# Performance work log

Measured on AMD Instinct MI355X. Metric: run time of the kernel, lower is better.

Reference implementation:

```python
import jax, jax.numpy as jnp
import numpy as np

TIME = 4096
DIM = 2048
DT_TAU = 0.1 / 1.0  # dt / tau


def setup_inputs() -> dict:
    key = jax.random.key(0)
    k1, k2, k3, k4 = jax.random.split(key, 4)
    inputs = jax.random.normal(k1, (TIME, 1, DIM), dtype=jnp.float32)
    W = jax.random.normal(k2, (DIM, DIM), dtype=jnp.float32) * 0.02  # recurrent weight (nn.Linear, bias=False)
    bias = jax.random.normal(k3, (1, DIM), dtype=jnp.float32)
    initial = jax.random.normal(k4, (1, DIM), dtype=jnp.float32)
    return {"inputs": inputs, "W": W, "bias": bias, "initial": initial}


def reference(inputs, W, bias, initial):
    # states[0] = initial; states[t+1] = s*(1-dt/tau) + (dt/tau)*(sigmoid(s+bias)@W.T + inputs[t])
    def step(state, x_t):
        f = jax.nn.sigmoid(state + bias) @ W.T  # [1, dim]
        new_state = state * (1.0 - DT_TAU) + DT_TAU * (f + x_t)
        return new_state, new_state

    _, rest = jax.lax.scan(step, initial, inputs[: TIME - 1])  # rest: [time-1, 1, dim]
    return jnp.concatenate([initial[None], rest], axis=0)  # [time, 1, dim]
```

## Files before the change

### kernel.cpp

```cpp
#include <hip/hip_runtime.h>
#include <hip/hip_fp16.h>
#include <hip/hip_cooperative_groups.h>
#include <stdint.h>

#define TIME_STEPS 4096
#define DIM        2048
#define NBLK       256
#define NTH        512
#define NWORK      32
#define WVB        8
#define RPW        8
#define PITCH      132

typedef uint32_t u32x4 __attribute__((ext_vector_type(4)));
typedef _Float16 h2f16 __attribute__((ext_vector_type(2)));


__device__ __forceinline__ uint32_t umin32(uint32_t a, uint32_t b) { return a < b ? a : b; }

__device__ __forceinline__ float dot2f(uint32_t packed, h2f16 w, float acc) {
#if __has_builtin(__builtin_amdgcn_fdot2)
  return __builtin_amdgcn_fdot2(__builtin_bit_cast(h2f16, packed), w, acc, false);
#else
  h2f16 a = __builtin_bit_cast(h2f16, packed);
  acc = fmaf((float)a.x, (float)w.x, acc);
  return fmaf((float)a.y, (float)w.y, acc);
#endif
}

template<int NSLOT>
__global__ __launch_bounds__(NTH, 2) void ctrnn_kernel(
    const float* __restrict__ x,
    const float* __restrict__ W,
    const float* __restrict__ bias,
    const float* __restrict__ initial,
    float* __restrict__ out,
    uint32_t* __restrict__ actbuf,
    uint32_t* __restrict__ progress,
    uint32_t* __restrict__ xccmap)
{
  const int tid  = threadIdx.x;
  const int lane = tid & 63;
  const int wv   = tid >> 6;

  if (tid == 0) {
    uint32_t xcc;
    asm volatile("s_getreg_b32 %0, hwreg(HW_REG_XCC_ID)" : "=s"(xcc));
    __hip_atomic_store(&xccmap[blockIdx.x], xcc,
                       __ATOMIC_RELAXED, __HIP_MEMORY_SCOPE_AGENT);
  }
  cooperative_groups::this_grid().sync();

  __shared__ uint32_t s_map[NBLK];
  for (int i = tid; i < NBLK; i += NTH)
    s_map[i] = __hip_atomic_load(&xccmap[i], __ATOMIC_RELAXED, __HIP_MEMORY_SCOPE_AGENT);
  __syncthreads();
  const uint32_t target = s_map[0];
  int before = 0, total = 0, beforeN = 0;
  const int bid = blockIdx.x;
  for (int i = 0; i < NBLK; ++i) {
    const bool m = (s_map[i] == target);
    total += m;
    if (i < bid) { before += m; beforeN += !m; }
  }
  const bool mine = (s_map[bid] == target);
  const int rank = mine ? before : (total + beforeN);
  if (rank >= NWORK) return;
  const int wb = rank;

  __shared__ uint32_t lds[2][16 * PITCH];

  const int gwid = wb * WVB + wv;
  const int row0 = gwid * RPW;

  const int s_c = lane >> 2, rr = lane & 3;
  const int cb  = s_c * 128 + rr * 4;
  h2f16 w2[RPW][16];
  #pragma unroll
  for (int m = 0; m < RPW; ++m) {
    const float* wr = W + (size_t)(row0 + m) * DIM + cb;
    #pragma unroll
    for (int k = 0; k < 8; ++k) {
      w2[m][2*k]   = h2f16{(_Float16)wr[k*16 + 0], (_Float16)wr[k*16 + 1]};
      w2[m][2*k+1] = h2f16{(_Float16)wr[k*16 + 2], (_Float16)wr[k*16 + 3]};
    }
  }

  float v = 0.f, bj = 0.f, xv = 0.f, xw = 0.f;
  if (lane < RPW) {
    const int j = row0 + lane;
    v  = initial[j];
    bj = bias[j];
    xv = x[j];
    xw = x[DIM + j];
    out[j] = v;
    const float a0 = 1.0f / (1.0f + __expf(-(v + bj)));
    __half h = __float2half_rn(a0);
    uint16_t hb; __builtin_memcpy(&hb, &h, 2);
    __hip_atomic_store(&actbuf[j], (1u << 16) | hb,
                       __ATOMIC_RELAXED, __HIP_MEMORY_SCOPE_AGENT);
  }

  const int e0   = wv * 256 + lane * 4;
  const int dstw = (e0 >> 7) * PITCH + (e0 & 127);

  uint32_t prog_seen = 0;

  for (int t = 0; t < TIME_STEPS - 1; ++t) {
    const int b = t & 1;
    const uint32_t needtag = (uint32_t)(t + 1);
    const uint32_t thresh  = needtag << 16;

    const uint32_t* qsrc = actbuf + (size_t)(t & (NSLOT - 1)) * DIM + e0;
    u32x4 q;
    for (;;) {
      asm volatile("global_load_dwordx4 %0, %1, off sc1\n\t"
                   "s_waitcnt vmcnt(0)"
                   : "=v"(q) : "v"(qsrc) : "memory");
      const uint32_t mn = umin32(umin32(q[0], q[1]), umin32(q[2], q[3]));
      if (mn >= thresh) break;
    }
    *reinterpret_cast<u32x4*>(&lds[b][dstw]) = q;

    __syncthreads();

    if (tid == 0)
      __hip_atomic_store(&progress[wb], needtag,
                         __ATOMIC_RELAXED, __HIP_MEMORY_SCOPE_AGENT);

    float xn = 0.f;
    if (lane < RPW && t + 2 < TIME_STEPS) xn = x[(size_t)(t + 2) * DIM + row0 + lane];

    float a0 = 0.f, a1 = 0.f, a2 = 0.f, a3 = 0.f;
    float a4 = 0.f, a5 = 0.f, a6 = 0.f, a7 = 0.f;
    #pragma unroll
    for (int k = 0; k < 8; ++k) {
      const u32x4 qq = *reinterpret_cast<const u32x4*>(
          &lds[b][s_c * PITCH + rr * 4 + k * 16]);
      const uint32_t lo = __builtin_amdgcn_perm(qq[1], qq[0], 0x05040100u);
      const uint32_t hi = __builtin_amdgcn_perm(qq[3], qq[2], 0x05040100u);
      a0 = dot2f(lo, w2[0][2*k], a0); a0 = dot2f(hi, w2[0][2*k+1], a0);
      a1 = dot2f(lo, w2[1][2*k], a1); a1 = dot2f(hi, w2[1][2*k+1], a1);
      a2 = dot2f(lo, w2[2][2*k], a2); a2 = dot2f(hi, w2[2][2*k+1], a2);
      a3 = dot2f(lo, w2[3][2*k], a3); a3 = dot2f(hi, w2[3][2*k+1], a3);
      a4 = dot2f(lo, w2[4][2*k], a4); a4 = dot2f(hi, w2[4][2*k+1], a4);
      a5 = dot2f(lo, w2[5][2*k], a5); a5 = dot2f(hi, w2[5][2*k+1], a5);
      a6 = dot2f(lo, w2[6][2*k], a6); a6 = dot2f(hi, w2[6][2*k+1], a6);
      a7 = dot2f(lo, w2[7][2*k], a7); a7 = dot2f(hi, w2[7][2*k+1], a7);
    }

    const float t0 = a0 + __shfl_xor(a0, 1, 64);
    const float t1 = a1 + __shfl_xor(a1, 1, 64);
    const float t2 = a2 + __shfl_xor(a2, 1, 64);
    const float t3 = a3 + __shfl_xor(a3, 1, 64);
    const float t4 = a4 + __shfl_xor(a4, 1, 64);
    const float t5 = a5 + __shfl_xor(a5, 1, 64);
    const float t6 = a6 + __shfl_xor(a6, 1, 64);
    const float t7 = a7 + __shfl_xor(a7, 1, 64);
    float b0 = (lane & 1) ? t1 : t0;
    float b1 = (lane & 1) ? t3 : t2;
    float b2 = (lane & 1) ? t5 : t4;
    float b3 = (lane & 1) ? t7 : t6;
    b0 += __shfl_xor(b0, 2, 64);
    b1 += __shfl_xor(b1, 2, 64);
    b2 += __shfl_xor(b2, 2, 64);
    b3 += __shfl_xor(b3, 2, 64);
    float c0 = (lane & 2) ? b1 : b0;
    float c1 = (lane & 2) ? b3 : b2;
    c0 += __shfl_xor(c0, 4, 64);
    c1 += __shfl_xor(c1, 4, 64);
    float p = (lane & 4) ? c1 : c0;
    p += __shfl_xor(p, 8, 64);
    p += __shfl_xor(p, 16, 64);
    p += __shfl_xor(p, 32, 64);

    if (t >= NSLOT - 1) {
      const uint32_t need = (uint32_t)(t + 2 - NSLOT);
      if (need > prog_seen) {
        for (;;) {
          uint32_t mn = __hip_atomic_load(&progress[lane & (NWORK - 1)],
                            __ATOMIC_RELAXED, __HIP_MEMORY_SCOPE_AGENT);
          uint32_t qv;
          qv = (uint32_t)__shfl_xor((int)mn, 1, 64);  mn = umin32(mn, qv);
          qv = (uint32_t)__shfl_xor((int)mn, 2, 64);  mn = umin32(mn, qv);
          qv = (uint32_t)__shfl_xor((int)mn, 4, 64);  mn = umin32(mn, qv);
          qv = (uint32_t)__shfl_xor((int)mn, 8, 64);  mn = umin32(mn, qv);
          qv = (uint32_t)__shfl_xor((int)mn, 16, 64); mn = umin32(mn, qv);
          if (mn >= need) { prog_seen = mn; break; }
        }
      }
    }

    if (lane < RPW) {
      v  = 0.9f * v + 0.1f * (p + xv);
      xv = xw;
      xw = xn;
      out[(size_t)(t + 1) * DIM + row0 + lane] = v;
      const float a = 1.0f / (1.0f + __expf(-(v + bj)));
      __half h = __float2half_rn(a);
      uint16_t hb; __builtin_memcpy(&hb, &h, 2);
      const uint32_t e = ((uint32_t)(t + 2) << 16) | hb;
      __hip_atomic_store(&actbuf[(size_t)((t + 1) & (NSLOT - 1)) * DIM + row0 + lane], e,
                         __ATOMIC_RELAXED, __HIP_MEMORY_SCOPE_AGENT);
    }
  }
}

extern "C" void kernel_launch(void* const* d_in, const int* in_sizes, int n_in,
                              void* d_out, int out_size, void* d_ws, size_t ws_size,
                              hipStream_t stream) {
  const float* x       = (const float*)d_in[0];
  const float* W       = (const float*)d_in[1];
  const float* bias    = (const float*)d_in[2];
  const float* initial = (const float*)d_in[3];
  float* out           = (float*)d_out;

  uint32_t* actbuf = (uint32_t*)d_ws;

  const size_t need8 = ((size_t)8 * DIM + NWORK + NBLK) * 4;
  void* kfun;
  size_t ringwords;
  if (ws_size >= need8) { kfun = (void*)ctrnn_kernel<8>; ringwords = (size_t)8 * DIM; }
  else                  { kfun = (void*)ctrnn_kernel<2>; ringwords = (size_t)2 * DIM; }

  uint32_t* progress = actbuf + ringwords;
  uint32_t* xccmap   = progress + NWORK;

  hipMemsetAsync(d_ws, 0, (ringwords + NWORK + NBLK) * 4, stream);

  void* args[] = { (void*)&x, (void*)&W, (void*)&bias, (void*)&initial,
                   (void*)&out, (void*)&actbuf, (void*)&progress, (void*)&xccmap };
  hipLaunchCooperativeKernel(kfun, dim3(NBLK), dim3(NTH), args, 0, stream);
}
```

Measured before the change: 9.271 ms.

## Add global epoch counter gate and repack activations with swizzled LDS layout

Adds a global epoch counter that is incremented once all wavefronts of all 32 worker blocks have published their step. Each step now spins on this single counter before polling the tagged activation ring, so the per-element poll should succeed on the first read and the polling traffic drops. The activations are also packed to fp16 pairs before the LDS store, using an XOR-swizzled layout instead of a padded pitch. Each lane then reads one contiguous 32-column slice of the packed activations, with the W register layout changed to match. The extra global atomic plus the vmcnt wait add latency to every step's critical path.

```diff
diff --git a/kernel.cpp b/kernel.cpp
--- a/kernel.cpp
+++ b/kernel.cpp
@@ -10,7 +10,6 @@
 #define NWORK      32
 #define WVB        8
 #define RPW        8
-#define PITCH      132
 
 typedef uint32_t u32x4 __attribute__((ext_vector_type(4)));
 typedef _Float16 h2f16 __attribute__((ext_vector_type(2)));
@@ -28,6 +27,8 @@
 #endif
 }
 
+__device__ __forceinline__ int swz(int p) { return p ^ (((p >> 5) & 7) << 2); }
+
 template<int NSLOT>
 __global__ __launch_bounds__(NTH, 2) void ctrnn_kernel(
     const float* __restrict__ x,
@@ -37,7 +38,8 @@
     float* __restrict__ out,
     uint32_t* __restrict__ actbuf,
     uint32_t* __restrict__ progress,
-    uint32_t* __restrict__ xccmap)
+    uint32_t* __restrict__ xccmap,
+    uint32_t* __restrict__ epoch)
 {
   const int tid  = threadIdx.x;
   const int lane = tid & 63;
@@ -68,22 +70,21 @@
   if (rank >= NWORK) return;
   const int wb = rank;
 
-  __shared__ uint32_t lds[2][16 * PITCH];
+  __shared__ uint32_t lds[2][1024];
+  __shared__ uint32_t prod_ctr;
+  if (tid == 0) prod_ctr = 0;
+  __syncthreads();
 
   const int gwid = wb * WVB + wv;
   const int row0 = gwid * RPW;
 
-  const int s_c = lane >> 2, rr = lane & 3;
-  const int cb  = s_c * 128 + rr * 4;
   h2f16 w2[RPW][16];
   #pragma unroll
   for (int m = 0; m < RPW; ++m) {
-    const float* wr = W + (size_t)(row0 + m) * DIM + cb;
+    const float* wr = W + (size_t)(row0 + m) * DIM + lane * 32;
     #pragma unroll
-    for (int k = 0; k < 8; ++k) {
-      w2[m][2*k]   = h2f16{(_Float16)wr[k*16 + 0], (_Float16)wr[k*16 + 1]};
-      w2[m][2*k+1] = h2f16{(_Float16)wr[k*16 + 2], (_Float16)wr[k*16 + 3]};
-    }
+    for (int q = 0; q < 16; ++q)
+      w2[m][q] = h2f16{(_Float16)wr[2*q], (_Float16)wr[2*q+1]};
   }
 
   float v = 0.f, bj = 0.f, xv = 0.f, xw = 0.f;
@@ -101,8 +102,8 @@
                        __ATOMIC_RELAXED, __HIP_MEMORY_SCOPE_AGENT);
   }
 
-  const int e0   = wv * 256 + lane * 4;
-  const int dstw = (e0 >> 7) * PITCH + (e0 & 127);
+  const int e0 = wv * 256 + lane * 4;
+  const int p0 = e0 >> 1;
 
   uint32_t prog_seen = 0;
 
@@ -110,6 +111,10 @@
     const int b = t & 1;
     const uint32_t needtag = (uint32_t)(t + 1);
     const uint32_t thresh  = needtag << 16;
+
+    const uint32_t etarget = 32u * (uint32_t)t;
+    while (__hip_atomic_load(epoch, __ATOMIC_RELAXED, __HIP_MEMORY_SCOPE_AGENT)
+           < etarget) { }
 
     const uint32_t* qsrc = actbuf + (size_t)(t & (NSLOT - 1)) * DIM + e0;
     u32x4 q;
@@ -120,7 +125,14 @@
       const uint32_t mn = umin32(umin32(q[0], q[1]), umin32(q[2], q[3]));
       if (mn >= thresh) break;
     }
-    *reinterpret_cast<u32x4*>(&lds[b][dstw]) = q;
+
+    {
+      const uint32_t lo = __builtin_amdgcn_perm(q[1], q[0], 0x05040100u);
+      const uint32_t hi = __builtin_amdgcn_perm(q[3], q[2], 0x05040100u);
+      const int w0 = swz(p0);
+      lds[b][w0]     = lo;
+      lds[b][w0 + 1] = hi;
+    }
 
     __syncthreads();
 
@@ -134,19 +146,21 @@
     float a0 = 0.f, a1 = 0.f, a2 = 0.f, a3 = 0.f;
     float a4 = 0.f, a5 = 0.f, a6 = 0.f, a7 = 0.f;
     #pragma unroll
-    for (int k = 0; k < 8; ++k) {
-      const u32x4 qq = *reinterpret_cast<const u32x4*>(
-          &lds[b][s_c * PITCH + rr * 4 + k * 16]);
-      const uint32_t lo = __builtin_amdgcn_perm(qq[1], qq[0], 0x05040100u);
-      const uint32_t hi = __builtin_amdgcn_perm(qq[3], qq[2], 0x05040100u);
-      a0 = dot2f(lo, w2[0][2*k], a0); a0 = dot2f(hi, w2[0][2*k+1], a0);
-      a1 = dot2f(lo, w2[1][2*k], a1); a1 = dot2f(hi, w2[1][2*k+1], a1);
-      a2 = dot2f(lo, w2[2][2*k], a2); a2 = dot2f(hi, w2[2][2*k+1], a2);
-      a3 = dot2f(lo, w2[3][2*k], a3); a3 = dot2f(hi, w2[3][2*k+1], a3);
-      a4 = dot2f(lo, w2[4][2*k], a4); a4 = dot2f(hi, w2[4][2*k+1], a4);
-      a5 = dot2f(lo, w2[5][2*k], a5); a5 = dot2f(hi, w2[5][2*k+1], a5);
-      a6 = dot2f(lo, w2[6][2*k], a6); a6 = dot2f(hi, w2[6][2*k+1], a6);
-      a7 = dot2f(lo, w2[7][2*k], a7); a7 = dot2f(hi, w2[7][2*k+1], a7);
+    for (int j = 0; j < 4; ++j) {
+      const u32x4 qq = *reinterpret_cast<const u32x4*>(&lds[b][swz(lane * 16 + 4 * j)]);
+      #pragma unroll
+      for (int i = 0; i < 4; ++i) {
+        const uint32_t pr = qq[i];
+        const int idx = 4 * j + i;
+        a0 = dot2f(pr, w2[0][idx], a0);
+        a1 = dot2f(pr, w2[1][idx], a1);
+        a2 = dot2f(pr, w2[2][idx], a2);
+        a3 = dot2f(pr, w2[3][idx], a3);
+        a4 = dot2f(pr, w2[4][idx], a4);
+        a5 = dot2f(pr, w2[5][idx], a5);
+        a6 = dot2f(pr, w2[6][idx], a6);
+        a7 = dot2f(pr, w2[7][idx], a7);
+      }
     }
 
     const float t0 = a0 + __shfl_xor(a0, 1, 64);
@@ -203,6 +217,13 @@
       __hip_atomic_store(&actbuf[(size_t)((t + 1) & (NSLOT - 1)) * DIM + row0 + lane], e,
                          __ATOMIC_RELAXED, __HIP_MEMORY_SCOPE_AGENT);
     }
+
+    asm volatile("s_waitcnt vmcnt(0)" ::: "memory");
+    if (lane == 0) {
+      const uint32_t old = atomicAdd(&prod_ctr, 1u);
+      if (old == 8u * (uint32_t)t + 7u)
+        __hip_atomic_fetch_add(epoch, 1u, __ATOMIC_RELAXED, __HIP_MEMORY_SCOPE_AGENT);
+    }
   }
 }
 
@@ -217,7 +238,7 @@
 
   uint32_t* actbuf = (uint32_t*)d_ws;
 
-  const size_t need8 = ((size_t)8 * DIM + NWORK + NBLK) * 4;
+  const size_t need8 = ((size_t)8 * DIM + NWORK + NBLK + 1) * 4;
   void* kfun;
   size_t ringwords;
   if (ws_size >= need8) { kfun = (void*)ctrnn_kernel<8>; ringwords = (size_t)8 * DIM; }
@@ -225,10 +246,12 @@
 
   uint32_t* progress = actbuf + ringwords;
   uint32_t* xccmap   = progress + NWORK;
-
-  hipMemsetAsync(d_ws, 0, (ringwords + NWORK + NBLK) * 4, stream);
+  uint32_t* epoch    = xccmap + NBLK;
+
+  hipMemsetAsync(d_ws, 0, (ringwords + NWORK + NBLK + 1) * 4, stream);
 
   void* args[] = { (void*)&x, (void*)&W, (void*)&bias, (void*)&initial,
-                   (void*)&out, (void*)&actbuf, (void*)&progress, (void*)&xccmap };
+                   (void*)&out, (void*)&actbuf, (void*)&progress,
+                   (void*)&xccmap, (void*)&epoch };
   hipLaunchCooperativeKernel(kfun, dim3(NBLK), dim3(NTH), args, 0, stream);
 }
```

After: 27.49 ms. 2.97x slower.
